# Performance work log

Hardware: AMD Instinct MI355X
Metric: run time of the kernel (lower is better)

The kernel has to match this reference:

```python
import jax, jax.numpy as jnp
import numpy as np

N, E, IN_DIM, OUT_DIM, T = 100000, 1600000, 128, 64, 8
V_THRESHOLD = 1.0
EPS = 1e-7

# ---- Lorentz manifold (curvature -1), time coordinate first ----

def _linner(a, b):
    # Lorentzian inner product <a,b>_L = -a0*b0 + sum_i ai*bi
    return -a[..., 0] * b[..., 0] + jnp.sum(a[..., 1:] * b[..., 1:], axis=-1)

def _proju(z, u):
    # project ambient vector u to tangent space at z (<z,z>_L = -1)
    return u + _linner(z, u)[..., None] * z

def _expmap(z, u):
    un = jnp.sqrt(jnp.maximum(_linner(u, u), EPS))[..., None]
    return jnp.cosh(un) * z + jnp.sinh(un) * u / un

def _dist0(z):
    # geodesic distance to origin o=(1,0,...,0): arccosh(-<o,z>_L) = arccosh(z0)
    return jnp.arccosh(jnp.maximum(z[..., 0], 1.0 + EPS))

# ---- GCNConv (torch_geometric semantics: self-loops + symmetric norm) ----

def _gcn(x, edge_index, W, b):
    src, dst = edge_index[0], edge_index[1]
    loops = jnp.arange(N, dtype=src.dtype)
    src = jnp.concatenate([src, loops])
    dst = jnp.concatenate([dst, loops])
    deg = jax.ops.segment_sum(jnp.ones_like(dst, dtype=x.dtype), dst, num_segments=N)
    dinv = jax.lax.rsqrt(jnp.maximum(deg, 1.0))  # deg >= 1 due to self-loops
    norm = dinv[src] * dinv[dst]                 # [E+N]
    h = x @ W                                    # [N, OUT_DIM]
    out = jax.ops.segment_sum(norm[:, None] * h[src], dst, num_segments=N)
    return out + b


def setup_inputs() -> dict:
    key = jax.random.key(0)
    k1, k2, k3 = jax.random.split(key, 3)
    x = jax.random.normal(k1, (N, IN_DIM), dtype=jnp.float32)
    edge_index = jax.random.randint(k2, (2, E), 0, N, dtype=jnp.int32)
    W = jax.random.normal(k3, (IN_DIM, OUT_DIM), dtype=jnp.float32) / np.sqrt(IN_DIM)
    b = jnp.zeros((OUT_DIM,), dtype=jnp.float32)
    return {"x": x, "edge_index": edge_index, "W": W, "b": b}


def reference(x, edge_index, W, b):
    h = _gcn(x, edge_index, W, b)                       # [N, D]
    origin = jnp.zeros_like(h).at[..., 0].set(1.0)      # manifold origin
    x_seq = jnp.broadcast_to(h, (T,) + h.shape)         # [T, N, D]

    def step(z, x_t):
        u = _proju(z, x_t)                              # input current in T_z M
        z_new = _expmap(z, u)                           # charge along geodesic
        v = _dist0(z_new)                               # membrane potential [N]
        spike = v >= V_THRESHOLD
        z_out = jnp.where(spike[..., None], origin, z_new)  # hard reset
        return z_out, (spike.astype(h.dtype), z_out)

    _, (o_seq, z_seq) = jax.lax.scan(step, origin, x_seq)
    return o_seq, z_seq  # [T, N], [T, N, D]
```

## Files before the change

kernel.cpp:

```cpp
#include <hip/hip_runtime.h>
#include <math.h>

#define IN_DIM_C 128
#define OUT_DIM_C 64
#define T_STEPS 8
#define KC_MAX 512
#define PTILE 2048
#define GKC 32

__device__ __forceinline__ float4 f4zero() { return make_float4(0.f, 0.f, 0.f, 0.f); }

__global__ __launch_bounds__(256) void k_hist(const int* __restrict__ dst,
                                              int* __restrict__ chist, int E) {
    __shared__ int hh[KC_MAX];
    const int tid = threadIdx.x;
    for (int i = tid; i < KC_MAX; i += 256) hh[i] = 0;
    __syncthreads();
    long base = (long)blockIdx.x * 4096;
    #pragma unroll
    for (int j = 0; j < 16; ++j) {
        long e = base + j * 256 + tid;
        if (e < E) atomicAdd(&hh[dst[e] >> 8], 1);
    }
    __syncthreads();
    for (int i = tid; i < KC_MAX; i += 256)
        if (hh[i]) atomicAdd(&chist[i], hh[i]);
}

__global__ __launch_bounds__(64) void k_scanK(const int* __restrict__ chist,
                                              int* __restrict__ gcursor,
                                              int* __restrict__ offsets,
                                              int kc, int n, int E) {
    int lane = threadIdx.x;
    int carry = 0;
    for (int c = 0; c * 64 < kc; ++c) {
        int idx = c * 64 + lane;
        int v = (idx < kc) ? chist[idx] : 0;
        int x = v;
        #pragma unroll
        for (int off = 1; off < 64; off <<= 1) {
            int t = __shfl_up(x, off, 64);
            if (lane >= off) x += t;
        }
        if (idx < kc) gcursor[idx] = carry + x - v;
        carry += __shfl(x, 63, 64);
    }
    if (lane == 0) offsets[n] = E;
}

__global__ __launch_bounds__(256) void k_gemm(const float* __restrict__ x,
                                              const float* __restrict__ W,
                                              float* __restrict__ h, int n) {
    __shared__ __align__(16) float xs[GKC * 132];
    __shared__ __align__(16) float Ws[GKC * OUT_DIM_C];

    const int tid = threadIdx.x;
    const int cg = tid & 7;
    const int ng = tid >> 3;
    const int node_base = blockIdx.x * 128;

    float acc[4][8];
    #pragma unroll
    for (int i = 0; i < 4; ++i)
        #pragma unroll
        for (int j = 0; j < 8; ++j) acc[i][j] = 0.f;

    #pragma unroll 1
    for (int c = 0; c < IN_DIM_C / GKC; ++c) {
        __syncthreads();
        #pragma unroll
        for (int i = 0; i < 4; ++i) {
            int idx = tid + i * 256;
            int nd = idx >> 3, k4 = idx & 7;
            int node = node_base + nd;
            float4 v = f4zero();
            if (node < n) v = *(const float4*)&x[(long)node * IN_DIM_C + c * GKC + k4 * 4];
            xs[(k4 * 4 + 0) * 132 + nd] = v.x;
            xs[(k4 * 4 + 1) * 132 + nd] = v.y;
            xs[(k4 * 4 + 2) * 132 + nd] = v.z;
            xs[(k4 * 4 + 3) * 132 + nd] = v.w;
        }
        #pragma unroll
        for (int i = 0; i < 2; ++i) {
            int idx = tid + i * 256;
            ((float4*)Ws)[idx] = ((const float4*)&W[c * GKC * OUT_DIM_C])[idx];
        }
        __syncthreads();

        #pragma unroll
        for (int k = 0; k < GKC; ++k) {
            float4 a = *(const float4*)&xs[k * 132 + ng * 4];
            const float* wr = &Ws[k * OUT_DIM_C + cg * 8];
            float4 b0 = *(const float4*)&wr[0];
            float4 b1 = *(const float4*)&wr[4];
            #pragma unroll
            for (int i = 0; i < 4; ++i) {
                float av = (i == 0) ? a.x : (i == 1) ? a.y : (i == 2) ? a.z : a.w;
                acc[i][0] = fmaf(av, b0.x, acc[i][0]);
                acc[i][1] = fmaf(av, b0.y, acc[i][1]);
                acc[i][2] = fmaf(av, b0.z, acc[i][2]);
                acc[i][3] = fmaf(av, b0.w, acc[i][3]);
                acc[i][4] = fmaf(av, b1.x, acc[i][4]);
                acc[i][5] = fmaf(av, b1.y, acc[i][5]);
                acc[i][6] = fmaf(av, b1.z, acc[i][6]);
                acc[i][7] = fmaf(av, b1.w, acc[i][7]);
            }
        }
    }

    #pragma unroll
    for (int i = 0; i < 4; ++i) {
        int node = node_base + ng * 4 + i;
        if (node < n) {
            *(float4*)&h[(long)node * OUT_DIM_C + cg * 8] =
                make_float4(acc[i][0], acc[i][1], acc[i][2], acc[i][3]);
            *(float4*)&h[(long)node * OUT_DIM_C + cg * 8 + 4] =
                make_float4(acc[i][4], acc[i][5], acc[i][6], acc[i][7]);
        }
    }
}

__global__ __launch_bounds__(256) void k_part(const int* __restrict__ src,
                                              const int* __restrict__ dst,
                                              int* __restrict__ gcursor,
                                              int* __restrict__ part, int E, int kc) {
    __shared__ int hist[KC_MAX];
    __shared__ int offs[KC_MAX];
    __shared__ int cur[KC_MAX];
    __shared__ int gbase[KC_MAX];
    const int tid = threadIdx.x;
    long base = (long)blockIdx.x * PTILE;

    for (int i = tid; i < KC_MAX; i += 256) hist[i] = 0;
    __syncthreads();
    #pragma unroll
    for (int j = 0; j < PTILE / 256; ++j) {
        long e = base + j * 256 + tid;
        if (e < E) atomicAdd(&hist[dst[e] >> 8], 1);
    }
    __syncthreads();
    if (tid < 64) {
        int carry = 0;
        for (int c = 0; c * 64 < kc; ++c) {
            int idx = c * 64 + tid;
            int v = (idx < kc) ? hist[idx] : 0;
            int x = v;
            #pragma unroll
            for (int off = 1; off < 64; off <<= 1) {
                int t = __shfl_up(x, off, 64);
                if (tid >= off) x += t;
            }
            if (idx < kc) { offs[idx] = carry + x - v; cur[idx] = carry + x - v; }
            carry += __shfl(x, 63, 64);
        }
    }
    __syncthreads();
    for (int b = tid; b < kc; b += 256)
        gbase[b] = hist[b] ? atomicAdd(&gcursor[b], hist[b]) : 0;
    __syncthreads();
    #pragma unroll
    for (int j = 0; j < PTILE / 256; ++j) {
        long e = base + j * 256 + tid;
        if (e < E) {
            int d = dst[e];
            int b = d >> 8;
            int r = atomicAdd(&cur[b], 1);
            part[gbase[b] + r - offs[b]] = (src[e] << 8) | (d & 255);
        }
    }
}

__global__ __launch_bounds__(256) void k_sort(const int* __restrict__ part,
                                              const int* __restrict__ gcursor,
                                              int* __restrict__ part2,
                                              int* __restrict__ offsets,
                                              float* __restrict__ dinv, int n) {
    __shared__ int cnt[256];
    __shared__ int cur[256];
    __shared__ int wsum[4], woff[4];
    const int tid = threadIdx.x;
    const int bkt = blockIdx.x;
    int start = bkt ? gcursor[bkt - 1] : 0;
    int end = gcursor[bkt];

    cnt[tid] = 0;
    __syncthreads();
    for (int i = start + tid; i < end; i += 256)
        atomicAdd(&cnt[part[i] & 255], 1);
    __syncthreads();

    int v = cnt[tid];
    int lane = tid & 63, wv = tid >> 6;
    int x = v;
    #pragma unroll
    for (int off = 1; off < 64; off <<= 1) {
        int t = __shfl_up(x, off, 64);
        if (lane >= off) x += t;
    }
    if (lane == 63) wsum[wv] = x;
    __syncthreads();
    if (tid == 0) { int c = 0; for (int w = 0; w < 4; ++w) { woff[w] = c; c += wsum[w]; } }
    __syncthreads();
    int myloc = woff[wv] + x - v;
    cur[tid] = myloc;
    int node = (bkt << 8) + tid;
    if (node < n) {
        offsets[node] = start + myloc;
        dinv[node] = rsqrtf((float)(v + 1));
    }
    __syncthreads();

    for (int i = start + tid; i < end; i += 256) {
        int p = part[i];
        int r = atomicAdd(&cur[p & 255], 1);
        part2[start + r] = ((unsigned)p) >> 8;
    }
}

__global__ __launch_bounds__(256) void k_pull(const int* __restrict__ offsets,
                                              const int* __restrict__ part2,
                                              const float* __restrict__ dinv,
                                              const float* __restrict__ h,
                                              const float* __restrict__ b,
                                              float* __restrict__ agg, int n) {
    int node = (blockIdx.x * 256 + threadIdx.x) >> 6;
    int lane = threadIdx.x & 63;
    if (node >= n) return;
    int o0 = offsets[node], o1 = offsets[node + 1];
    float dd = dinv[node];
    float acc = fmaf(dd * dd, h[(long)node * OUT_DIM_C + lane], b[lane]);
    int i = o0;
    for (; i + 4 <= o1; i += 4) {
        int s0 = part2[i], s1 = part2[i + 1], s2 = part2[i + 2], s3 = part2[i + 3];
        float n0 = dinv[s0] * dd, n1 = dinv[s1] * dd, n2 = dinv[s2] * dd, n3 = dinv[s3] * dd;
        acc = fmaf(n0, h[(long)s0 * OUT_DIM_C + lane], acc);
        acc = fmaf(n1, h[(long)s1 * OUT_DIM_C + lane], acc);
        acc = fmaf(n2, h[(long)s2 * OUT_DIM_C + lane], acc);
        acc = fmaf(n3, h[(long)s3 * OUT_DIM_C + lane], acc);
    }
    for (; i < o1; ++i) {
        int s = part2[i];
        acc = fmaf(dinv[s] * dd, h[(long)s * OUT_DIM_C + lane], acc);
    }
    agg[(long)node * OUT_DIM_C + lane] = acc;
}

__global__ __launch_bounds__(256) void k_spike(const float* agg,
                                               float* o_seq, float* z_seq, int n) {
    int gid = blockIdx.x * 256 + threadIdx.x;
    int node = gid >> 4;
    int sub = threadIdx.x & 15;
    if (node >= n) return;
    const float s0 = (sub == 0) ? -1.0f : 1.0f;
    int lane0 = (threadIdx.x & 63) & ~15;

    float4 g = *(const float4*)&agg[(long)node * OUT_DIM_C + sub * 4];
    float4 origin = f4zero();
    if (sub == 0) origin.x = 1.0f;

    auto step = [&](float4 z, float4& zn, bool& sp) {
        float p = s0 * z.x * g.x + z.y * g.y + z.z * g.z + z.w * g.w;
        p += __shfl_xor(p, 1, 64);
        p += __shfl_xor(p, 2, 64);
        p += __shfl_xor(p, 4, 64);
        p += __shfl_xor(p, 8, 64);
        float4 u = make_float4(fmaf(p, z.x, g.x), fmaf(p, z.y, g.y),
                               fmaf(p, z.z, g.z), fmaf(p, z.w, g.w));
        float q = s0 * u.x * u.x + u.y * u.y + u.z * u.z + u.w * u.w;
        q += __shfl_xor(q, 1, 64);
        q += __shfl_xor(q, 2, 64);
        q += __shfl_xor(q, 4, 64);
        q += __shfl_xor(q, 8, 64);
        float un = sqrtf(fmaxf(q, 1e-7f));
        float c = coshf(un);
        float sh = sinhf(un) / un;
        zn = make_float4(fmaf(c, z.x, sh * u.x), fmaf(c, z.y, sh * u.y),
                         fmaf(c, z.z, sh * u.z), fmaf(c, z.w, sh * u.w));
        float z0 = __shfl(zn.x, lane0, 64);
        float v = acoshf(fmaxf(z0, 1.0f + 1e-7f));
        sp = (v >= 1.0f);
    };

    float4 z1; bool sp0;
    step(origin, z1, sp0);
    float4 r0 = sp0 ? origin : z1;

    float4 z = origin;
    bool at0 = true;
    for (int t = 0; t < T_STEPS; ++t) {
        float4 zn; bool sp;
        if (at0) { sp = sp0; zn = r0; }
        else {
            step(z, zn, sp);
            if (sp) zn = origin;
        }
        *(float4*)&z_seq[(long)t * n * OUT_DIM_C + (long)node * OUT_DIM_C + sub * 4] = zn;
        if (sub == 0) o_seq[(long)t * n + node] = sp ? 1.0f : 0.0f;
        z = zn;
        at0 = sp;
    }
}

extern "C" void kernel_launch(void* const* d_in, const int* in_sizes, int n_in,
                              void* d_out, int out_size, void* d_ws, size_t ws_size,
                              hipStream_t stream) {
    const float* x  = (const float*)d_in[0];
    const int*   ei = (const int*)d_in[1];
    const float* W  = (const float*)d_in[2];
    const float* b  = (const float*)d_in[3];
    const int N = in_sizes[0] / IN_DIM_C;
    const int E = in_sizes[1] / 2;
    const int KC = (N + 255) >> 8;

    float* out   = (float*)d_out;
    float* o_seq = out;
    float* z_seq = out + (long)T_STEPS * N;

    float* agg     = z_seq;
    float* h       = z_seq + 1L * N * OUT_DIM_C;
    int*   part    = (int*)(z_seq + 2L * N * OUT_DIM_C);
    int*   part2   = (int*)(z_seq + 3L * N * OUT_DIM_C);
    int*   chist   = (int*)(z_seq + 4L * N * OUT_DIM_C);
    int*   gcursor = chist + KC_MAX;
    int*   offsets = gcursor + KC_MAX;
    float* dinv    = (float*)(offsets + N + 1);

    const int* srcp = ei;
    const int* dstp = ei + E;

    hipMemsetAsync(chist, 0, (size_t)KC_MAX * sizeof(int), stream);
    k_hist<<<(E + 4095) / 4096, 256, 0, stream>>>(dstp, chist, E);
    k_scanK<<<1, 64, 0, stream>>>(chist, gcursor, offsets, KC, N, E);

    k_gemm<<<(N + 127) / 128, 256, 0, stream>>>(x, W, h, N);

    k_part<<<(E + PTILE - 1) / PTILE, 256, 0, stream>>>(srcp, dstp, gcursor, part, E, KC);
    k_sort<<<KC, 256, 0, stream>>>(part, gcursor, part2, offsets, dinv, N);
    k_pull<<<(N * 64 + 255) / 256, 256, 0, stream>>>(offsets, part2, dinv, h, b, agg, N);

    k_spike<<<(N + 15) / 16, 256, 0, stream>>>(agg, o_seq, z_seq, N);
}
```

Measured before the change: 415.2 us.

## Fuse neighbor aggregation into spike kernel using workspace buffers

Merges the GCN pull-aggregation with the Lorentz spiking recurrence so each node's aggregated feature stays in registers instead of being written to and re-read from global memory. Intermediate buffers (h, sorted edges, offsets, dinv) move into the workspace so they do not alias z_seq, which the fused kernel writes. The gather now uses 16 lanes per node with float4 loads rather than 64 scalar lanes. The old path is kept as a fallback when the workspace is too small.

```diff
diff --git a/kernel.cpp b/kernel.cpp
--- a/kernel.cpp
+++ b/kernel.cpp
@@ -217,36 +217,13 @@
     }
 }
 
-__global__ __launch_bounds__(256) void k_pull(const int* __restrict__ offsets,
-                                              const int* __restrict__ part2,
-                                              const float* __restrict__ dinv,
-                                              const float* __restrict__ h,
-                                              const float* __restrict__ b,
-                                              float* __restrict__ agg, int n) {
-    int node = (blockIdx.x * 256 + threadIdx.x) >> 6;
-    int lane = threadIdx.x & 63;
-    if (node >= n) return;
-    int o0 = offsets[node], o1 = offsets[node + 1];
-    float dd = dinv[node];
-    float acc = fmaf(dd * dd, h[(long)node * OUT_DIM_C + lane], b[lane]);
-    int i = o0;
-    for (; i + 4 <= o1; i += 4) {
-        int s0 = part2[i], s1 = part2[i + 1], s2 = part2[i + 2], s3 = part2[i + 3];
-        float n0 = dinv[s0] * dd, n1 = dinv[s1] * dd, n2 = dinv[s2] * dd, n3 = dinv[s3] * dd;
-        acc = fmaf(n0, h[(long)s0 * OUT_DIM_C + lane], acc);
-        acc = fmaf(n1, h[(long)s1 * OUT_DIM_C + lane], acc);
-        acc = fmaf(n2, h[(long)s2 * OUT_DIM_C + lane], acc);
-        acc = fmaf(n3, h[(long)s3 * OUT_DIM_C + lane], acc);
-    }
-    for (; i < o1; ++i) {
-        int s = part2[i];
-        acc = fmaf(dinv[s] * dd, h[(long)s * OUT_DIM_C + lane], acc);
-    }
-    agg[(long)node * OUT_DIM_C + lane] = acc;
-}
-
-__global__ __launch_bounds__(256) void k_spike(const float* agg,
-                                               float* o_seq, float* z_seq, int n) {
+__global__ __launch_bounds__(256) void k_pullspike(const int* __restrict__ offsets,
+                                                   const int* __restrict__ part2,
+                                                   const float* __restrict__ dinv,
+                                                   const float* __restrict__ h,
+                                                   const float* __restrict__ b,
+                                                   float* __restrict__ o_seq,
+                                                   float* __restrict__ z_seq, int n) {
     int gid = blockIdx.x * 256 + threadIdx.x;
     int node = gid >> 4;
     int sub = threadIdx.x & 15;
@@ -254,7 +231,39 @@
     const float s0 = (sub == 0) ? -1.0f : 1.0f;
     int lane0 = (threadIdx.x & 63) & ~15;
 
-    float4 g = *(const float4*)&agg[(long)node * OUT_DIM_C + sub * 4];
+    int o0 = offsets[node], o1 = offsets[node + 1];
+    float dd = dinv[node];
+    float4 hv = *(const float4*)&h[(long)node * OUT_DIM_C + sub * 4];
+    float4 bv = *(const float4*)&b[sub * 4];
+    float dd2 = dd * dd;
+    float4 g = make_float4(fmaf(dd2, hv.x, bv.x), fmaf(dd2, hv.y, bv.y),
+                           fmaf(dd2, hv.z, bv.z), fmaf(dd2, hv.w, bv.w));
+    int i = o0;
+    for (; i + 4 <= o1; i += 4) {
+        int s0i = part2[i], s1i = part2[i + 1], s2i = part2[i + 2], s3i = part2[i + 3];
+        float w0 = dinv[s0i] * dd, w1 = dinv[s1i] * dd;
+        float w2 = dinv[s2i] * dd, w3 = dinv[s3i] * dd;
+        float4 h0 = *(const float4*)&h[(long)s0i * OUT_DIM_C + sub * 4];
+        float4 h1 = *(const float4*)&h[(long)s1i * OUT_DIM_C + sub * 4];
+        float4 h2 = *(const float4*)&h[(long)s2i * OUT_DIM_C + sub * 4];
+        float4 h3 = *(const float4*)&h[(long)s3i * OUT_DIM_C + sub * 4];
+        g.x = fmaf(w0, h0.x, g.x); g.y = fmaf(w0, h0.y, g.y);
+        g.z = fmaf(w0, h0.z, g.z); g.w = fmaf(w0, h0.w, g.w);
+        g.x = fmaf(w1, h1.x, g.x); g.y = fmaf(w1, h1.y, g.y);
+        g.z = fmaf(w1, h1.z, g.z); g.w = fmaf(w1, h1.w, g.w);
+        g.x = fmaf(w2, h2.x, g.x); g.y = fmaf(w2, h2.y, g.y);
+        g.z = fmaf(w2, h2.z, g.z); g.w = fmaf(w2, h2.w, g.w);
+        g.x = fmaf(w3, h3.x, g.x); g.y = fmaf(w3, h3.y, g.y);
+        g.z = fmaf(w3, h3.z, g.z); g.w = fmaf(w3, h3.w, g.w);
+    }
+    for (; i < o1; ++i) {
+        int s = part2[i];
+        float w = dinv[s] * dd;
+        float4 h0 = *(const float4*)&h[(long)s * OUT_DIM_C + sub * 4];
+        g.x = fmaf(w, h0.x, g.x); g.y = fmaf(w, h0.y, g.y);
+        g.z = fmaf(w, h0.z, g.z); g.w = fmaf(w, h0.w, g.w);
+    }
+
     float4 origin = f4zero();
     if (sub == 0) origin.x = 1.0f;
 
@@ -301,6 +310,92 @@
     }
 }
 
+__global__ __launch_bounds__(256) void k_pull(const int* __restrict__ offsets,
+                                              const int* __restrict__ part2,
+                                              const float* __restrict__ dinv,
+                                              const float* __restrict__ h,
+                                              const float* __restrict__ b,
+                                              float* __restrict__ agg, int n) {
+    int node = (blockIdx.x * 256 + threadIdx.x) >> 6;
+    int lane = threadIdx.x & 63;
+    if (node >= n) return;
+    int o0 = offsets[node], o1 = offsets[node + 1];
+    float dd = dinv[node];
+    float acc = fmaf(dd * dd, h[(long)node * OUT_DIM_C + lane], b[lane]);
+    int i = o0;
+    for (; i + 4 <= o1; i += 4) {
+        int s0 = part2[i], s1 = part2[i + 1], s2 = part2[i + 2], s3 = part2[i + 3];
+        float n0 = dinv[s0] * dd, n1 = dinv[s1] * dd, n2 = dinv[s2] * dd, n3 = dinv[s3] * dd;
+        acc = fmaf(n0, h[(long)s0 * OUT_DIM_C + lane], acc);
+        acc = fmaf(n1, h[(long)s1 * OUT_DIM_C + lane], acc);
+        acc = fmaf(n2, h[(long)s2 * OUT_DIM_C + lane], acc);
+        acc = fmaf(n3, h[(long)s3 * OUT_DIM_C + lane], acc);
+    }
+    for (; i < o1; ++i) {
+        int s = part2[i];
+        acc = fmaf(dinv[s] * dd, h[(long)s * OUT_DIM_C + lane], acc);
+    }
+    agg[(long)node * OUT_DIM_C + lane] = acc;
+}
+
+__global__ __launch_bounds__(256) void k_spike(const float* agg,
+                                               float* o_seq, float* z_seq, int n) {
+    int gid = blockIdx.x * 256 + threadIdx.x;
+    int node = gid >> 4;
+    int sub = threadIdx.x & 15;
+    if (node >= n) return;
+    const float s0 = (sub == 0) ? -1.0f : 1.0f;
+    int lane0 = (threadIdx.x & 63) & ~15;
+
+    float4 g = *(const float4*)&agg[(long)node * OUT_DIM_C + sub * 4];
+    float4 origin = f4zero();
+    if (sub == 0) origin.x = 1.0f;
+
+    auto step = [&](float4 z, float4& zn, bool& sp) {
+        float p = s0 * z.x * g.x + z.y * g.y + z.z * g.z + z.w * g.w;
+        p += __shfl_xor(p, 1, 64);
+        p += __shfl_xor(p, 2, 64);
+        p += __shfl_xor(p, 4, 64);
+        p += __shfl_xor(p, 8, 64);
+        float4 u = make_float4(fmaf(p, z.x, g.x), fmaf(p, z.y, g.y),
+                               fmaf(p, z.z, g.z), fmaf(p, z.w, g.w));
+        float q = s0 * u.x * u.x + u.y * u.y + u.z * u.z + u.w * u.w;
+        q += __shfl_xor(q, 1, 64);
+        q += __shfl_xor(q, 2, 64);
+        q += __shfl_xor(q, 4, 64);
+        q += __shfl_xor(q, 8, 64);
+        float un = sqrtf(fmaxf(q, 1e-7f));
+        float c = coshf(un);
+        float sh = sinhf(un) / un;
+        zn = make_float4(fmaf(c, z.x, sh * u.x), fmaf(c, z.y, sh * u.y),
+                         fmaf(c, z.z, sh * u.z), fmaf(c, z.w, sh * u.w));
+        float z0 = __shfl(zn.x, lane0, 64);
+        float v = acoshf(fmaxf(z0, 1.0f + 1e-7f));
+        sp = (v >= 1.0f);
+    };
+
+    float4 z1; bool sp0;
+    step(origin, z1, sp0);
+    float4 r0 = sp0 ? origin : z1;
+
+    float4 z = origin;
+    bool at0 = true;
+    for (int t = 0; t < T_STEPS; ++t) {
+        float4 zn; bool sp;
+        if (at0) { sp = sp0; zn = r0; }
+        else {
+            step(z, zn, sp);
+            if (sp) zn = origin;
+        }
+        *(float4*)&z_seq[(long)t * n * OUT_DIM_C + (long)node * OUT_DIM_C + sub * 4] = zn;
+        if (sub == 0) o_seq[(long)t * n + node] = sp ? 1.0f : 0.0f;
+        z = zn;
+        at0 = sp;
+    }
+}
+
+static inline size_t align256(size_t x) { return (x + 255) & ~(size_t)255; }
+
 extern "C" void kernel_launch(void* const* d_in, const int* in_sizes, int n_in,
                               void* d_out, int out_size, void* d_ws, size_t ws_size,
                               hipStream_t stream) {
@@ -316,27 +411,55 @@
     float* o_seq = out;
     float* z_seq = out + (long)T_STEPS * N;
 
-    float* agg     = z_seq;
-    float* h       = z_seq + 1L * N * OUT_DIM_C;
-    int*   part    = (int*)(z_seq + 2L * N * OUT_DIM_C);
-    int*   part2   = (int*)(z_seq + 3L * N * OUT_DIM_C);
-    int*   chist   = (int*)(z_seq + 4L * N * OUT_DIM_C);
-    int*   gcursor = chist + KC_MAX;
-    int*   offsets = gcursor + KC_MAX;
-    float* dinv    = (float*)(offsets + N + 1);
-
     const int* srcp = ei;
     const int* dstp = ei + E;
 
-    hipMemsetAsync(chist, 0, (size_t)KC_MAX * sizeof(int), stream);
-    k_hist<<<(E + 4095) / 4096, 256, 0, stream>>>(dstp, chist, E);
-    k_scanK<<<1, 64, 0, stream>>>(chist, gcursor, offsets, KC, N, E);
-
-    k_gemm<<<(N + 127) / 128, 256, 0, stream>>>(x, W, h, N);
-
-    k_part<<<(E + PTILE - 1) / PTILE, 256, 0, stream>>>(srcp, dstp, gcursor, part, E, KC);
-    k_sort<<<KC, 256, 0, stream>>>(part, gcursor, part2, offsets, dinv, N);
-    k_pull<<<(N * 64 + 255) / 256, 256, 0, stream>>>(offsets, part2, dinv, h, b, agg, N);
-
-    k_spike<<<(N + 15) / 16, 256, 0, stream>>>(agg, o_seq, z_seq, N);
-}
+    size_t off_h    = 0;
+    size_t off_p2   = align256(off_h + (size_t)N * OUT_DIM_C * 4);
+    size_t off_offs = align256(off_p2 + (size_t)E * 4);
+    size_t off_dinv = align256(off_offs + (size_t)(N + 1) * 4);
+    size_t need     = align256(off_dinv + (size_t)N * 4);
+
+    if (d_ws != nullptr && ws_size >= need) {
+        float* h       = (float*)((char*)d_ws + off_h);
+        int*   part2   = (int*)((char*)d_ws + off_p2);
+        int*   offsets = (int*)((char*)d_ws + off_offs);
+        float* dinv    = (float*)((char*)d_ws + off_dinv);
+        int*   part    = (int*)(z_seq + 0L * N * OUT_DIM_C);
+        int*   chist   = (int*)(z_seq + 1L * N * OUT_DIM_C);
+        int*   gcursor = chist + KC_MAX;
+
+        hipMemsetAsync(chist, 0, (size_t)KC_MAX * sizeof(int), stream);
+        k_hist<<<(E + 4095) / 4096, 256, 0, stream>>>(dstp, chist, E);
+        k_scanK<<<1, 64, 0, stream>>>(chist, gcursor, offsets, KC, N, E);
+
+        k_gemm<<<(N + 127) / 128, 256, 0, stream>>>(x, W, h, N);
+
+        k_part<<<(E + PTILE - 1) / PTILE, 256, 0, stream>>>(srcp, dstp, gcursor, part, E, KC);
+        k_sort<<<KC, 256, 0, stream>>>(part, gcursor, part2, offsets, dinv, N);
+
+        k_pullspike<<<(N + 15) / 16, 256, 0, stream>>>(offsets, part2, dinv, h, b,
+                                                       o_seq, z_seq, N);
+    } else {
+        float* agg     = z_seq;
+        float* h       = z_seq + 1L * N * OUT_DIM_C;
+        int*   part    = (int*)(z_seq + 2L * N * OUT_DIM_C);
+        int*   part2   = (int*)(z_seq + 3L * N * OUT_DIM_C);
+        int*   chist   = (int*)(z_seq + 4L * N * OUT_DIM_C);
+        int*   gcursor = chist + KC_MAX;
+        int*   offsets = gcursor + KC_MAX;
+        float* dinv    = (float*)(offsets + N + 1);
+
+        hipMemsetAsync(chist, 0, (size_t)KC_MAX * sizeof(int), stream);
+        k_hist<<<(E + 4095) / 4096, 256, 0, stream>>>(dstp, chist, E);
+        k_scanK<<<1, 64, 0, stream>>>(chist, gcursor, offsets, KC, N, E);
+
+        k_gemm<<<(N + 127) / 128, 256, 0, stream>>>(x, W, h, N);
+
+        k_part<<<(E + PTILE - 1) / PTILE, 256, 0, stream>>>(srcp, dstp, gcursor, part, E, KC);
+        k_sort<<<KC, 256, 0, stream>>>(part, gcursor, part2, offsets, dinv, N);
+        k_pull<<<(N * 64 + 255) / 256, 256, 0, stream>>>(offsets, part2, dinv, h, b, agg, N);
+
+        k_spike<<<(N + 15) / 16, 256, 0, stream>>>(agg, o_seq, z_seq, N);
+    }
+}
```

Measured after the change: 405.2 us. 1.02x faster.
